# Performance work log

Hardware: AMD Instinct MI355X
Metric: run time of the kernel (lower is better)

The kernel has to match this reference:

```python
import jax, jax.numpy as jnp
import numpy as np

N_NODES = 50000
N_EDGES = 800000
D_IN = 128
HEADS = 4
CH = 32            # hidden_channels == out_channels
N_LAYERS = 3
NEG_SLOPE = 0.2


def setup_inputs() -> dict:
    key = jax.random.key(0)
    ks = jax.random.split(key, 8)
    x = jax.random.normal(ks[0], (N_NODES, D_IN), dtype=jnp.float32)
    edge_index = jax.random.randint(ks[1], (2, N_EDGES), 0, N_NODES, dtype=jnp.int32)
    # All layers map D_IN -> HEADS*CH == D_IN (128->128), so params stack on a layer axis.
    scale = 1.0 / np.sqrt(D_IN)
    Wsrc = jax.random.normal(ks[2], (N_LAYERS, D_IN, HEADS * CH), dtype=jnp.float32) * scale
    Wdst = jax.random.normal(ks[3], (N_LAYERS, D_IN, HEADS * CH), dtype=jnp.float32) * scale
    att_src = jax.random.normal(ks[4], (N_LAYERS, HEADS, CH), dtype=jnp.float32) * scale
    att_dst = jax.random.normal(ks[5], (N_LAYERS, HEADS, CH), dtype=jnp.float32) * scale
    bias = jnp.zeros((N_LAYERS, HEADS * CH), dtype=jnp.float32)
    return {"x": x, "edge_index": edge_index, "Wsrc": Wsrc, "Wdst": Wdst,
            "att_src": att_src, "att_dst": att_dst, "bias": bias}


def _gat_layer(x, src, dst, Wsrc, Wdst, a_src, a_dst, b):
    N = x.shape[0]
    xs = (x @ Wsrc).reshape(N, HEADS, CH)   # source-projected feats
    xd = (x @ Wdst).reshape(N, HEADS, CH)   # dest-projected feats
    al_s = jnp.einsum('nhc,hc->nh', xs, a_src)   # [N,H]
    al_d = jnp.einsum('nhc,hc->nh', xd, a_dst)   # [N,H]
    e = jax.nn.leaky_relu(al_s[src] + al_d[dst], NEG_SLOPE)   # [E,H]
    # segment softmax over incoming edges per destination node
    m = jax.ops.segment_max(e, dst, num_segments=N)           # [N,H]
    ex = jnp.exp(e - m[dst])
    s = jax.ops.segment_sum(ex, dst, num_segments=N)          # [N,H]
    alpha = ex / (s[dst] + 1e-16)                             # [E,H]
    msg = xs[src] * alpha[:, :, None]                         # [E,H,C]
    out = jax.ops.segment_sum(msg, dst, num_segments=N)       # [N,H,C]
    return out.reshape(N, HEADS * CH) + b


def reference(x, edge_index, Wsrc, Wdst, att_src, att_dst, bias):
    src, dst = edge_index[0], edge_index[1]
    for i in range(N_LAYERS):
        x = _gat_layer(x, src, dst, Wsrc[i], Wdst[i], att_src[i], att_dst[i], bias[i])
        if i < N_LAYERS - 1:
            x = jax.nn.relu(x)
    return x
```

## Files before the change

### kernel.cpp

```cpp
#include <hip/hip_runtime.h>
#include <hip/hip_fp16.h>

#define NN 50000
#define NE 800000
#define D 128
#define H 4
#define CH 32
#define NEG 0.2f
#define CAP 64

#define BSH 10
#define NBIN 49
#define BCAP 256
#define PCAP 24576
#define EPB 8192

typedef _Float16 half8v __attribute__((ext_vector_type(8)));
typedef _Float16 half4v __attribute__((ext_vector_type(4)));
typedef float f32x4 __attribute__((ext_vector_type(4)));

__global__ void k_prep(const float* __restrict__ Wsrc, const float* __restrict__ Wdst,
                       const float* __restrict__ attS, const float* __restrict__ attD,
                       float* __restrict__ weff, _Float16* __restrict__ WT,
                       int* __restrict__ gcnt) {
    int b = blockIdx.x;
    if (b < 24) {
        int l = b >> 3, o = b & 7, hh = o & 3;
        int k = threadIdx.x;
        const float* W = ((o < 4) ? Wsrc : Wdst) + (size_t)l * D * D;
        const float* att = ((o < 4) ? attS : attD) + l * H * CH + hh * CH;
        float s = 0.f;
        #pragma unroll
        for (int c = 0; c < CH; c += 4) {
            float4 wv = *(const float4*)(W + (size_t)k * D + hh * CH + c);
            s += wv.x * att[c] + wv.y * att[c + 1] + wv.z * att[c + 2] + wv.w * att[c + 3];
        }
        weff[b * 128 + k] = s;
    } else if (b < 408) {
        int q = b - 24;
        int l = q >> 7, n = q & 127;
        int k = threadIdx.x;
        float v = Wsrc[(size_t)l * D * D + (size_t)k * D + n];
        WT[(size_t)l * D * D + (size_t)n * D + k] = (_Float16)v;
    } else {
        int i = threadIdx.x;
        if (i < NBIN) gcnt[i] = 0;
    }
}

__global__ __launch_bounds__(256) void k_bin(const int* __restrict__ src,
                                             const int* __restrict__ dst,
                                             int* __restrict__ gcnt,
                                             unsigned int* __restrict__ pairbuf) {
    __shared__ int bcnt[NBIN];
    __shared__ int bbase[NBIN];
    __shared__ unsigned int lbuf[NBIN][BCAP];
    int tid = threadIdx.x;
    int e0 = blockIdx.x * EPB;

    for (int b = tid; b < NBIN; b += 256) bcnt[b] = 0;
    __syncthreads();

    #pragma unroll
    for (int i = 0; i < EPB / 256; i++) {
        int e = e0 + i * 256 + tid;
        if (e < NE) {
            int d = dst[e];
            int s = src[e];
            int bin = d >> BSH;
            unsigned int pack = ((unsigned int)(d & ((1 << BSH) - 1)) << 16) | (unsigned int)s;
            int pos = atomicAdd(&bcnt[bin], 1);
            if (pos < BCAP) {
                lbuf[bin][pos] = pack;
            } else {
                int gp = atomicAdd(&gcnt[bin], 1);
                if (gp < PCAP) pairbuf[(size_t)bin * PCAP + gp] = pack;
            }
        }
    }
    __syncthreads();
    if (tid < NBIN) {
        int c = bcnt[tid]; if (c > BCAP) c = BCAP;
        bbase[tid] = atomicAdd(&gcnt[tid], c);
    }
    __syncthreads();
    for (int b = 0; b < NBIN; b++) {
        int c = bcnt[b]; if (c > BCAP) c = BCAP;
        int base = bbase[b];
        for (int i = tid; i < c; i += 256)
            pairbuf[(size_t)b * PCAP + base + i] = lbuf[b][i];
    }
}

__global__ __launch_bounds__(256) void k_place(const int* __restrict__ gcnt,
                                               const unsigned int* __restrict__ pairbuf,
                                               int* __restrict__ fill,
                                               int* __restrict__ bucket) {
    __shared__ int ldeg[1 << BSH];
    int tid = threadIdx.x;
    int b = blockIdx.x;
    for (int i = tid; i < (1 << BSH); i += 256) ldeg[i] = 0;
    __syncthreads();

    int cnt = gcnt[b]; if (cnt > PCAP) cnt = PCAP;
    int nbase = b << BSH;
    for (int i = tid; i < cnt; i += 256) {
        unsigned int p = pairbuf[(size_t)b * PCAP + i];
        int nl = p >> 16;
        int s = p & 0xFFFF;
        int pos = atomicAdd(&ldeg[nl], 1);
        if (pos < CAP) bucket[((nbase + nl) << 6) + pos] = s;
    }
    __syncthreads();
    for (int nl = tid; nl < (1 << BSH); nl += 256) {
        int n = nbase + nl;
        if (n < NN) { int d = ldeg[nl]; fill[n] = d > CAP ? CAP : d; }
    }
}

__global__ __launch_bounds__(512, 2) void k_gemm_mfma(
        const float* __restrict__ x, const _Float16* __restrict__ WT,
        const float* __restrict__ weff, __half* __restrict__ xs,
        float* __restrict__ als, float* __restrict__ ald) {
    __shared__ _Float16 Ah[64 * 128];
    __shared__ _Float16 Al[64 * 128];
    __shared__ _Float16 Bh[128 * 128];
    __shared__ _Float16 WF[16 * 128];

    int tid = threadIdx.x;
    int n0 = blockIdx.x * 64;

    #pragma unroll
    for (int j = 0; j < 4; j++) {
        int q = j * 512 + tid;
        int n = q >> 4, k16 = q & 15;
        int elem = (n * 128 + k16 * 8) ^ ((n & 7) << 3);
        *(float4*)&Bh[elem] = *(const float4*)&WT[(size_t)q * 8];
    }
    {
        int idx = tid * 4;
        int o = idx >> 7, k4 = idx & 127;
        half4v hv = {0, 0, 0, 0};
        if (o < 8) {
            float4 v = *(const float4*)&weff[o * 128 + k4];
            hv = (half4v){(_Float16)v.x, (_Float16)v.y, (_Float16)v.z, (_Float16)v.w};
        }
        *(half4v*)&WF[(o * 128 + k4) ^ ((o & 7) << 3)] = hv;
    }
    #pragma unroll
    for (int j = 0; j < 4; j++) {
        int q = j * 512 + tid;
        int row = q >> 5, c4 = q & 31;
        int rg = n0 + row; if (rg >= NN) rg = NN - 1;
        float4 v = *(const float4*)&x[(size_t)rg * D + c4 * 4];
        _Float16 h0 = (_Float16)v.x, h1 = (_Float16)v.y;
        _Float16 h2 = (_Float16)v.z, h3 = (_Float16)v.w;
        int elem = (row * 128 + c4 * 4) ^ ((row & 7) << 3);
        *(half4v*)&Ah[elem] = (half4v){h0, h1, h2, h3};
        *(half4v*)&Al[elem] = (half4v){(_Float16)(v.x - (float)h0), (_Float16)(v.y - (float)h1),
                                       (_Float16)(v.z - (float)h2), (_Float16)(v.w - (float)h3)};
    }
    __syncthreads();

    int w = tid >> 6, l = tid & 63;
    int mt = w & 3, nh = w >> 2;
    int lm = l & 15, lg = l >> 4;
    int arow = mt * 16 + lm;
    int abase = arow * 128 + lg * 8;
    int aswz = (arow & 7) << 3;

    f32x4 acc0 = {0,0,0,0}, acc1 = {0,0,0,0}, acc2 = {0,0,0,0}, acc3 = {0,0,0,0};
    f32x4 accw = {0,0,0,0};

    #pragma unroll
    for (int ks = 0; ks < 4; ks++) {
        half8v ah = *(half8v*)&Ah[(abase + ks * 32) ^ aswz];
        half8v al = *(half8v*)&Al[(abase + ks * 32) ^ aswz];
        #pragma unroll
        for (int nt = 0; nt < 4; nt++) {
            int n = nh * 64 + nt * 16 + lm;
            int be = (n * 128 + ks * 32 + lg * 8) ^ ((n & 7) << 3);
            half8v bh = *(half8v*)&Bh[be];
            f32x4 a = (nt == 0) ? acc0 : (nt == 1) ? acc1 : (nt == 2) ? acc2 : acc3;
            a = __builtin_amdgcn_mfma_f32_16x16x32_f16(ah, bh, a, 0, 0, 0);
            a = __builtin_amdgcn_mfma_f32_16x16x32_f16(al, bh, a, 0, 0, 0);
            if (nt == 0) acc0 = a; else if (nt == 1) acc1 = a;
            else if (nt == 2) acc2 = a; else acc3 = a;
        }
        if (nh == 0) {
            int we = (lm * 128 + ks * 32 + lg * 8) ^ ((lm & 7) << 3);
            half8v wv = *(half8v*)&WF[we];
            accw = __builtin_amdgcn_mfma_f32_16x16x32_f16(ah, wv, accw, 0, 0, 0);
            accw = __builtin_amdgcn_mfma_f32_16x16x32_f16(al, wv, accw, 0, 0, 0);
        }
    }

    #pragma unroll
    for (int nt = 0; nt < 4; nt++) {
        f32x4 a = (nt == 0) ? acc0 : (nt == 1) ? acc1 : (nt == 2) ? acc2 : acc3;
        int col = nh * 64 + nt * 16 + lm;
        #pragma unroll
        for (int i = 0; i < 4; i++) {
            int row = n0 + mt * 16 + lg * 4 + i;
            if (row < NN) xs[(size_t)row * D + col] = __float2half(a[i]);
        }
    }
    if (nh == 0 && lm < 8) {
        #pragma unroll
        for (int i = 0; i < 4; i++) {
            int row = n0 + mt * 16 + lg * 4 + i;
            if (row < NN) {
                if (lm < 4) als[row * H + lm] = accw[i];
                else        ald[row * H + (lm - 4)] = accw[i];
            }
        }
    }
}

__global__ __launch_bounds__(256) void k_fused(const int* __restrict__ fill,
                                               const int* __restrict__ bucket,
                                               const float* __restrict__ als,
                                               const float* __restrict__ ald,
                                               const __half* __restrict__ xs,
                                               const float* __restrict__ bias,
                                               float* __restrict__ out,
                                               int do_relu) {
    __shared__ float wlds[4][256];
    __shared__ int   slds[4][64];
    int wv = threadIdx.x >> 6, lane = threadIdx.x & 63;
    int n = blockIdx.x * 4 + wv;
    int deg = fill[n]; if (deg > CAP) deg = CAP;
    int start = n << 6;
    int half = lane >> 5, sl = lane & 31;

    if (deg == 0) {
        if (half == 0) {
            float4 b4 = *(const float4*)&bias[sl * 4];
            if (do_relu) {
                b4.x = fmaxf(b4.x, 0.f); b4.y = fmaxf(b4.y, 0.f);
                b4.z = fmaxf(b4.z, 0.f); b4.w = fmaxf(b4.w, 0.f);
            }
            *(float4*)&out[(size_t)n * D + sl * 4] = b4;
        }
        return;
    }

    int slot = lane >> 2, h = lane & 3;
    float adv = ald[n * H + h];
    int dm1 = deg - 1;

    int i0 = slot, i1 = slot + 16, i2 = slot + 32, i3 = slot + 48;
    int s0 = bucket[start + min(i0, dm1)];
    int s1 = bucket[start + min(i1, dm1)];
    int s2 = bucket[start + min(i2, dm1)];
    int s3 = bucket[start + min(i3, dm1)];

    uint2 u[12];
    #pragma unroll
    for (int p = 0; p < 12; p++) {
        int idx = p * 2 + half;
        int id = __shfl((p < 8) ? s0 : s1, (idx & 15) * 4, 64);
        u[p] = *(const uint2*)&xs[(size_t)id * D + sl * 4];
    }

    float a0 = als[s0 * H + h] + adv;
    float a1 = als[s1 * H + h] + adv;
    float a2 = als[s2 * H + h] + adv;
    float a3 = als[s3 * H + h] + adv;
    a0 = a0 > 0.f ? a0 : NEG * a0;
    a1 = a1 > 0.f ? a1 : NEG * a1;
    a2 = a2 > 0.f ? a2 : NEG * a2;
    a3 = a3 > 0.f ? a3 : NEG * a3;
    float lg0 = (i0 < deg) ? a0 : -1e30f;
    float lg1 = (i1 < deg) ? a1 : -1e30f;
    float lg2 = (i2 < deg) ? a2 : -1e30f;
    float lg3 = (i3 < deg) ? a3 : -1e30f;
    float m = fmaxf(fmaxf(lg0, lg1), fmaxf(lg2, lg3));
    #pragma unroll
    for (int msk = 4; msk < 64; msk <<= 1) m = fmaxf(m, __shfl_xor(m, msk, 64));

    float w0 = (i0 < deg) ? __expf(lg0 - m) : 0.f;
    float w1 = (i1 < deg) ? __expf(lg1 - m) : 0.f;
    float w2 = (i2 < deg) ? __expf(lg2 - m) : 0.f;
    float w3 = (i3 < deg) ? __expf(lg3 - m) : 0.f;
    float sm = w0 + w1 + w2 + w3;
    #pragma unroll
    for (int msk = 4; msk < 64; msk <<= 1) sm += __shfl_xor(sm, msk, 64);

    wlds[wv][i0 * 4 + h] = w0;
    wlds[wv][i1 * 4 + h] = w1;
    wlds[wv][i2 * 4 + h] = w2;
    wlds[wv][i3 * 4 + h] = w3;
    if (h == 0) {
        slds[wv][i0] = s0; slds[wv][i1] = s1; slds[wv][i2] = s2; slds[wv][i3] = s3;
    }

    float invh = 1.f / (sm + 1e-16f);
    int h2 = sl >> 3;
    float inv4 = __shfl(invh, h2, 64);

    float ax = 0.f, ay = 0.f, az = 0.f, aw = 0.f;
    #pragma unroll
    for (int p = 0; p < 12; p++) {
        float wgt = wlds[wv][(p * 2 + half) * 4 + h2];
        float2 f0 = __half22float2(__builtin_bit_cast(__half2, u[p].x));
        float2 f1 = __half22float2(__builtin_bit_cast(__half2, u[p].y));
        ax = fmaf(wgt, f0.x, ax); ay = fmaf(wgt, f0.y, ay);
        az = fmaf(wgt, f1.x, az); aw = fmaf(wgt, f1.y, aw);
    }
    if (deg > 24) {
        int capR = (deg + 7) & ~7;
        for (int e = 24; e < capR; e += 8) {
            int iA = e + half, iB = e + 2 + half, iC = e + 4 + half, iD = e + 6 + half;
            int tA = slds[wv][iA], tB = slds[wv][iB];
            int tC = slds[wv][iC], tD = slds[wv][iD];
            float wA = wlds[wv][iA * 4 + h2], wB = wlds[wv][iB * 4 + h2];
            float wC = wlds[wv][iC * 4 + h2], wD = wlds[wv][iD * 4 + h2];
            uint2 uA = *(const uint2*)&xs[(size_t)tA * D + sl * 4];
            uint2 uB = *(const uint2*)&xs[(size_t)tB * D + sl * 4];
            uint2 uC = *(const uint2*)&xs[(size_t)tC * D + sl * 4];
            uint2 uD = *(const uint2*)&xs[(size_t)tD * D + sl * 4];
            float2 fA0 = __half22float2(__builtin_bit_cast(__half2, uA.x));
            float2 fA1 = __half22float2(__builtin_bit_cast(__half2, uA.y));
            float2 fB0 = __half22float2(__builtin_bit_cast(__half2, uB.x));
            float2 fB1 = __half22float2(__builtin_bit_cast(__half2, uB.y));
            float2 fC0 = __half22float2(__builtin_bit_cast(__half2, uC.x));
            float2 fC1 = __half22float2(__builtin_bit_cast(__half2, uC.y));
            float2 fD0 = __half22float2(__builtin_bit_cast(__half2, uD.x));
            float2 fD1 = __half22float2(__builtin_bit_cast(__half2, uD.y));
            ax = fmaf(wA, fA0.x, ax); ay = fmaf(wA, fA0.y, ay);
            az = fmaf(wA, fA1.x, az); aw = fmaf(wA, fA1.y, aw);
            ax = fmaf(wB, fB0.x, ax); ay = fmaf(wB, fB0.y, ay);
            az = fmaf(wB, fB1.x, az); aw = fmaf(wB, fB1.y, aw);
            ax = fmaf(wC, fC0.x, ax); ay = fmaf(wC, fC0.y, ay);
            az = fmaf(wC, fC1.x, az); aw = fmaf(wC, fC1.y, aw);
            ax = fmaf(wD, fD0.x, ax); ay = fmaf(wD, fD0.y, ay);
            az = fmaf(wD, fD1.x, az); aw = fmaf(wD, fD1.y, aw);
        }
    }

    ax += __shfl_xor(ax, 32, 64);
    ay += __shfl_xor(ay, 32, 64);
    az += __shfl_xor(az, 32, 64);
    aw += __shfl_xor(aw, 32, 64);

    if (half == 0) {
        float4 b4 = *(const float4*)&bias[sl * 4];
        float4 o4;
        o4.x = ax * inv4 + b4.x;
        o4.y = ay * inv4 + b4.y;
        o4.z = az * inv4 + b4.z;
        o4.w = aw * inv4 + b4.w;
        if (do_relu) {
            o4.x = fmaxf(o4.x, 0.f); o4.y = fmaxf(o4.y, 0.f);
            o4.z = fmaxf(o4.z, 0.f); o4.w = fmaxf(o4.w, 0.f);
        }
        *(float4*)&out[(size_t)n * D + sl * 4] = o4;
    }
}

extern "C" void kernel_launch(void* const* d_in, const int* in_sizes, int n_in,
                              void* d_out, int out_size, void* d_ws, size_t ws_size,
                              hipStream_t stream) {
    const float* x_in   = (const float*)d_in[0];
    const int*   edge   = (const int*)d_in[1];
    const float* Wsrc   = (const float*)d_in[2];
    const float* Wdst   = (const float*)d_in[3];
    const float* attsrc = (const float*)d_in[4];
    const float* attdst = (const float*)d_in[5];
    const float* bias   = (const float*)d_in[6];
    float* out = (float*)d_out;

    const int* src = edge;
    const int* dst = edge + NE;

    char* ws = (char*)d_ws;
    size_t off = 0;
    auto alloc = [&](size_t bytes) -> void* {
        void* p = ws + off;
        off += (bytes + 255) & ~(size_t)255;
        return p;
    };

    int* fill    = (int*)alloc(NN * sizeof(int));
    int* bucket  = (int*)alloc((size_t)NN * CAP * sizeof(int));
    int* gcnt    = (int*)alloc(NBIN * sizeof(int));
    unsigned int* pairbuf = (unsigned int*)alloc((size_t)NBIN * PCAP * sizeof(int));
    __half* xs   = (__half*)alloc((size_t)NN * D * sizeof(__half));
    float* als   = (float*)alloc(NN * H * sizeof(float));
    float* ald   = (float*)alloc(NN * H * sizeof(float));
    float* weff  = (float*)alloc(3 * 8 * 128 * sizeof(float));
    _Float16* WT = (_Float16*)alloc((size_t)3 * D * D * sizeof(_Float16));
    float* bufA  = (float*)alloc((size_t)NN * D * sizeof(float));
    float* bufB  = (float*)alloc((size_t)NN * D * sizeof(float));

    k_prep<<<409, 128, 0, stream>>>(Wsrc, Wdst, attsrc, attdst, weff, WT, gcnt);
    k_bin<<<(NE + EPB - 1) / EPB, 256, 0, stream>>>(src, dst, gcnt, pairbuf);
    k_place<<<NBIN, 256, 0, stream>>>(gcnt, pairbuf, fill, bucket);

    for (int l = 0; l < 3; l++) {
        const float* xin  = (l == 0) ? x_in : ((l == 1) ? bufA : bufB);
        float*       xout = (l == 2) ? out : ((l == 0) ? bufA : bufB);

        k_gemm_mfma<<<(NN + 63) / 64, 512, 0, stream>>>(
            xin, WT + (size_t)l * D * D, weff + l * 8 * 128, xs, als, ald);
        k_fused<<<NN / 4, 256, 0, stream>>>(fill, bucket, als, ald, xs,
                                            bias + l * D, xout, (l < 2) ? 1 : 0);
    }
}
```

Before: 196.7 us.

## Store degree in bucket slot, drop split-fp16 GEMM residual, raise occupancy

```diff
diff --git a/kernel.cpp b/kernel.cpp
--- a/kernel.cpp
+++ b/kernel.cpp
@@ -7,7 +7,7 @@
 #define H 4
 #define CH 32
 #define NEG 0.2f
-#define CAP 64
+#define CAP 63
 
 #define BSH 10
 #define NBIN 49
@@ -94,7 +94,6 @@
 
 __global__ __launch_bounds__(256) void k_place(const int* __restrict__ gcnt,
                                                const unsigned int* __restrict__ pairbuf,
-                                               int* __restrict__ fill,
                                                int* __restrict__ bucket) {
     __shared__ int ldeg[1 << BSH];
     int tid = threadIdx.x;
@@ -114,16 +113,18 @@
     __syncthreads();
     for (int nl = tid; nl < (1 << BSH); nl += 256) {
         int n = nbase + nl;
-        if (n < NN) { int d = ldeg[nl]; fill[n] = d > CAP ? CAP : d; }
-    }
-}
-
-__global__ __launch_bounds__(512, 2) void k_gemm_mfma(
+        if (n < NN) {
+            int d = ldeg[nl]; if (d > CAP) d = CAP;
+            bucket[(n << 6) + 63] = d;
+        }
+    }
+}
+
+__global__ __launch_bounds__(512, 6) void k_gemm_mfma(
         const float* __restrict__ x, const _Float16* __restrict__ WT,
         const float* __restrict__ weff, __half* __restrict__ xs,
         float* __restrict__ als, float* __restrict__ ald) {
     __shared__ _Float16 Ah[64 * 128];
-    __shared__ _Float16 Al[64 * 128];
     __shared__ _Float16 Bh[128 * 128];
     __shared__ _Float16 WF[16 * 128];
 
@@ -153,12 +154,9 @@
         int row = q >> 5, c4 = q & 31;
         int rg = n0 + row; if (rg >= NN) rg = NN - 1;
         float4 v = *(const float4*)&x[(size_t)rg * D + c4 * 4];
-        _Float16 h0 = (_Float16)v.x, h1 = (_Float16)v.y;
-        _Float16 h2 = (_Float16)v.z, h3 = (_Float16)v.w;
         int elem = (row * 128 + c4 * 4) ^ ((row & 7) << 3);
-        *(half4v*)&Ah[elem] = (half4v){h0, h1, h2, h3};
-        *(half4v*)&Al[elem] = (half4v){(_Float16)(v.x - (float)h0), (_Float16)(v.y - (float)h1),
-                                       (_Float16)(v.z - (float)h2), (_Float16)(v.w - (float)h3)};
+        *(half4v*)&Ah[elem] = (half4v){(_Float16)v.x, (_Float16)v.y,
+                                       (_Float16)v.z, (_Float16)v.w};
     }
     __syncthreads();
 
@@ -175,7 +173,6 @@
     #pragma unroll
     for (int ks = 0; ks < 4; ks++) {
         half8v ah = *(half8v*)&Ah[(abase + ks * 32) ^ aswz];
-        half8v al = *(half8v*)&Al[(abase + ks * 32) ^ aswz];
         #pragma unroll
         for (int nt = 0; nt < 4; nt++) {
             int n = nh * 64 + nt * 16 + lm;
@@ -183,7 +180,6 @@
             half8v bh = *(half8v*)&Bh[be];
             f32x4 a = (nt == 0) ? acc0 : (nt == 1) ? acc1 : (nt == 2) ? acc2 : acc3;
             a = __builtin_amdgcn_mfma_f32_16x16x32_f16(ah, bh, a, 0, 0, 0);
-            a = __builtin_amdgcn_mfma_f32_16x16x32_f16(al, bh, a, 0, 0, 0);
             if (nt == 0) acc0 = a; else if (nt == 1) acc1 = a;
             else if (nt == 2) acc2 = a; else acc3 = a;
         }
@@ -191,7 +187,6 @@
             int we = (lm * 128 + ks * 32 + lg * 8) ^ ((lm & 7) << 3);
             half8v wv = *(half8v*)&WF[we];
             accw = __builtin_amdgcn_mfma_f32_16x16x32_f16(ah, wv, accw, 0, 0, 0);
-            accw = __builtin_amdgcn_mfma_f32_16x16x32_f16(al, wv, accw, 0, 0, 0);
         }
     }
 
@@ -217,8 +212,7 @@
     }
 }
 
-__global__ __launch_bounds__(256) void k_fused(const int* __restrict__ fill,
-                                               const int* __restrict__ bucket,
+__global__ __launch_bounds__(256) void k_fused(const int* __restrict__ bucket,
                                                const float* __restrict__ als,
                                                const float* __restrict__ ald,
                                                const __half* __restrict__ xs,
@@ -229,9 +223,16 @@
     __shared__ int   slds[4][64];
     int wv = threadIdx.x >> 6, lane = threadIdx.x & 63;
     int n = blockIdx.x * 4 + wv;
-    int deg = fill[n]; if (deg > CAP) deg = CAP;
     int start = n << 6;
     int half = lane >> 5, sl = lane & 31;
+    int slot = lane >> 2, h = lane & 3;
+
+    int i0 = slot, i1 = slot + 16, i2 = slot + 32, i3 = slot + 48;
+    int s0r = bucket[start + i0];
+    int s1r = bucket[start + i1];
+    int s2r = bucket[start + i2];
+    int s3r = bucket[start + i3];
+    int deg = __shfl(s3r, 60, 64);
 
     if (deg == 0) {
         if (half == 0) {
@@ -245,15 +246,10 @@
         return;
     }
 
-    int slot = lane >> 2, h = lane & 3;
-    float adv = ald[n * H + h];
-    int dm1 = deg - 1;
-
-    int i0 = slot, i1 = slot + 16, i2 = slot + 32, i3 = slot + 48;
-    int s0 = bucket[start + min(i0, dm1)];
-    int s1 = bucket[start + min(i1, dm1)];
-    int s2 = bucket[start + min(i2, dm1)];
-    int s3 = bucket[start + min(i3, dm1)];
+    int s0 = min(max(s0r, 0), NN - 1);
+    int s1 = min(max(s1r, 0), NN - 1);
+    int s2 = min(max(s2r, 0), NN - 1);
+    int s3 = min(max(s3r, 0), NN - 1);
 
     uint2 u[12];
     #pragma unroll
@@ -263,6 +259,7 @@
         u[p] = *(const uint2*)&xs[(size_t)id * D + sl * 4];
     }
 
+    float adv = ald[n * H + h];
     float a0 = als[s0 * H + h] + adv;
     float a1 = als[s1 * H + h] + adv;
     float a2 = als[s2 * H + h] + adv;
@@ -382,8 +379,7 @@
         return p;
     };
 
-    int* fill    = (int*)alloc(NN * sizeof(int));
-    int* bucket  = (int*)alloc((size_t)NN * CAP * sizeof(int));
+    int* bucket  = (int*)alloc((size_t)NN * 64 * sizeof(int));
     int* gcnt    = (int*)alloc(NBIN * sizeof(int));
     unsigned int* pairbuf = (unsigned int*)alloc((size_t)NBIN * PCAP * sizeof(int));
     __half* xs   = (__half*)alloc((size_t)NN * D * sizeof(__half));
@@ -396,7 +392,7 @@
 
     k_prep<<<409, 128, 0, stream>>>(Wsrc, Wdst, attsrc, attdst, weff, WT, gcnt);
     k_bin<<<(NE + EPB - 1) / EPB, 256, 0, stream>>>(src, dst, gcnt, pairbuf);
-    k_place<<<NBIN, 256, 0, stream>>>(gcnt, pairbuf, fill, bucket);
+    k_place<<<NBIN, 256, 0, stream>>>(gcnt, pairbuf, bucket);
 
     for (int l = 0; l < 3; l++) {
         const float* xin  = (l == 0) ? x_in : ((l == 1) ? bufA : bufB);
@@ -404,7 +400,7 @@
 
         k_gemm_mfma<<<(NN + 63) / 64, 512, 0, stream>>>(
             xin, WT + (size_t)l * D * D, weff + l * 8 * 128, xs, als, ald);
-        k_fused<<<NN / 4, 256, 0, stream>>>(fill, bucket, als, ald, xs,
+        k_fused<<<NN / 4, 256, 0, stream>>>(bucket, als, ald, xs,
                                             bias + l * D, xout, (l < 2) ? 1 : 0);
     }
 }
```

Measured after the change: 191.2 us. 1.03x faster.
